# Kernel tuning notes

Measured on AMD Instinct MI355X. Metric: run time of the kernel, lower is better.

The kernel has to match this reference:

```python
import jax, jax.numpy as jnp
import numpy as np

NE = 14          # NUM_ELEMENTS
NC = 20          # world channels
CLONER = 13      # cloner element one-hot channel
CA = NE + 3      # cloner_assigns channel (=17)
B, H, W = 32, 256, 256

# torch.roll equivalents (dims 2 = H, dims 3 = W)
def _below(x):  return jnp.roll(x, -1, axis=2)
def _above(x):  return jnp.roll(x,  1, axis=2)
def _left(x):   return jnp.roll(x,  1, axis=3)
def _right(x):  return jnp.roll(x, -1, axis=3)
DIRS = (_below, _above, _left, _right)


def setup_inputs() -> dict:
    key = jax.random.key(0)
    k1, k2, k3, k4, k5 = jax.random.split(key, 5)
    # one-hot element channels [B, NE, H, W]
    ids = jax.random.randint(k1, (B, H, W), 0, NE)
    onehot = jnp.transpose(jax.nn.one_hot(ids, NE, dtype=jnp.float32), (0, 3, 1, 2))
    # extra scalar channels [B, NC-NE, H, W]
    extra = jax.random.normal(k2, (B, NC - NE, H, W), dtype=jnp.float32)
    world = jnp.concatenate([onehot, extra], axis=1)
    # cloner_assigns channel holds element ids stored as floats
    ca_init = jax.random.randint(k3, (B, 1, H, W), 0, NE).astype(jnp.float32)
    world = world.at[:, CA:CA + 1].set(ca_init)
    elem_vecs = jax.random.normal(k4, (NE, NC), dtype=jnp.float32)  # embedding table
    info = jax.random.normal(k5, (B,), dtype=jnp.float32)
    return {"world": world, "elem_vecs": elem_vecs, "info": info}


def _forward(world, elem_vecs):
    # labels = argmax over element one-hot channels, kept as [B,1,H,W]
    labels = jnp.argmax(world[:, :NE], axis=1)[:, None].astype(world.dtype)
    is_not_cloner = ~(world[:, CLONER:CLONER + 1] > 0.5)
    # Pass 1: sequentially propagate a label into empty cloner assignment slots.
    for d in DIRS:
        ca = world[:, CA:CA + 1]
        is_cloner_empty = (~is_not_cloner) & ((ca == 0.0) | (ca == 13.0))
        # torch: ~(is_cloner_empty|is_not_cloner)*ca + is_cloner_empty*dir_labels
        new_ca = jnp.where(is_cloner_empty, d(labels),
                           jnp.where(is_not_cloner, jnp.zeros((), world.dtype), ca))
        world = world.at[:, CA:CA + 1].set(new_ca)
    # Embedding lookup of assigned element vectors: [B,H,W,NC] -> [B,NC,H,W]
    vec = jnp.transpose(elem_vecs[world[:, CA].astype(jnp.int32)], (0, 3, 1, 2))
    # Pass 2: sequentially write cloner's element vector into adjacent empty cells.
    for d in DIRS:
        ca = world[:, CA:CA + 1]
        is_cloner = world[:, CLONER:CLONER + 1] > 0.5
        is_empty = world[:, 0:1] > 0.5
        mask = d(is_cloner & (ca != 0.0) & (ca != 13.0)) & is_empty  # [B,1,H,W]
        world = jnp.where(mask, d(vec), world)
    return world


def reference(world, elem_vecs, info):
    return (_forward(world, elem_vecs), info)
```

## Files before the change

### kernel.cpp

```cpp
#include <hip/hip_runtime.h>

namespace {
constexpr int kNE = 14;
constexpr int kNC = 20;
constexpr int kCloner = 13;
constexpr int kCA = 17;
constexpr int kB = 32;
constexpr int kH = 256;
constexpr int kW = 256;

constexpr int kSH = 4;
constexpr int kThreads = 256;
constexpr size_t kPlane = (size_t)kH * kW;

constexpr int kT = 32;
constexpr int kE = kT + 4;
constexpr int kLW = 40;
}


__global__ __launch_bounds__(kThreads)
void k_pack(const float* __restrict__ world, const float* __restrict__ info,
            float* __restrict__ out, unsigned char* __restrict__ pack)
{
    const int g = blockIdx.x * kThreads + threadIdx.x;
    const int b = g >> 14;
    const int rem = g & 16383;
    const size_t off = (size_t)rem << 2;
    const float* wb = world + (size_t)b * kNC * kPlane;

    int lab[4] = {0, 0, 0, 0};
    #pragma unroll
    for (int c = 0; c < kNE; ++c) {
        const float4 v = *reinterpret_cast<const float4*>(wb + (size_t)c * kPlane + off);
        if (v.x > 0.5f) lab[0] = c;
        if (v.y > 0.5f) lab[1] = c;
        if (v.z > 0.5f) lab[2] = c;
        if (v.w > 0.5f) lab[3] = c;
    }
    const float4 ca4 = *reinterpret_cast<const float4*>(wb + (size_t)kCA * kPlane + off);
    uchar4 p;
    p.x = (unsigned char)(lab[0] | ((int)ca4.x << 4));
    p.y = (unsigned char)(lab[1] | ((int)ca4.y << 4));
    p.z = (unsigned char)(lab[2] | ((int)ca4.z << 4));
    p.w = (unsigned char)(lab[3] | ((int)ca4.w << 4));
    *reinterpret_cast<uchar4*>(pack + (size_t)b * kPlane + off) = p;

    if (g < kB) out[(size_t)kB * kNC * kPlane + g] = info[g];
}

__device__ __forceinline__ unsigned bc_step(unsigned s, unsigned ns,
                                            const unsigned short* __restrict__ vb) {
    if ((ns & 2u) && (s & 1u)) {
        const unsigned v = (ns >> 4) & 15u;
        return (s & 0x00F0u) | vb[v] | (v << 8) | 0x1000u;
    }
    return s;
}

__global__ __launch_bounds__(kThreads)
void k_apply(const float* __restrict__ world, const float* __restrict__ ev,
             const unsigned char* __restrict__ pack, float* __restrict__ out)
{
    __shared__ unsigned char  sP[kSH + 4][kW];
    __shared__ unsigned short sA[kSH + 2][kW];
    __shared__ float sEV[kNE * kNC];
    __shared__ unsigned short sVbits[kNE];

    const int tid = threadIdx.x;
    const int y0 = blockIdx.x * kSH;
    const int b  = blockIdx.y;
    const float* wb = world + (size_t)b * kNC * kPlane;
    float*       ob = out   + (size_t)b * kNC * kPlane;
    const unsigned char* pb = pack + (size_t)b * kPlane;

    const int th   = tid >> 6;
    const int col4 = (tid & 63) * 4;
    const size_t off4 = (size_t)(y0 + th) * kW + col4;

    float4 extra[5];
    extra[0] = *reinterpret_cast<const float4*>(wb + (size_t)14 * kPlane + off4);
    extra[1] = *reinterpret_cast<const float4*>(wb + (size_t)15 * kPlane + off4);
    extra[2] = *reinterpret_cast<const float4*>(wb + (size_t)16 * kPlane + off4);
    extra[3] = *reinterpret_cast<const float4*>(wb + (size_t)18 * kPlane + off4);
    extra[4] = *reinterpret_cast<const float4*>(wb + (size_t)19 * kPlane + off4);

    for (int i = tid; i < kNE * kNC; i += kThreads) sEV[i] = ev[i];
    if (tid < kNE) {
        const float e0  = ev[tid * kNC + 0];
        const float c13 = ev[tid * kNC + kCloner];
        const float c17 = ev[tid * kNC + kCA];
        unsigned short vb = 0;
        if (e0 > 0.5f) vb |= 1;
        if (c13 > 0.5f && c17 != 0.0f && c17 != 13.0f) vb |= 2;
        sVbits[tid] = vb;
    }

    for (int idx = tid; idx < (kSH + 4) * (kW / 4); idx += kThreads) {
        const int r  = idx >> 6;
        const int c4 = (idx & 63) * 4;
        const int h  = (y0 - 2 + r) & (kH - 1);
        *reinterpret_cast<uchar4*>(&sP[r][c4]) =
            *reinterpret_cast<const uchar4*>(pb + (size_t)h * kW + c4);
    }
    __syncthreads();

    for (int idx = tid; idx < (kSH + 2) * kW; idx += kThreads) {
        const int r   = idx >> 8;
        const int col = idx & 255;
        const int pr  = r + 1;
        const unsigned p  = sP[pr][col];
        const unsigned lb = p & 15u;
        int fca = 0;
        if (lb == kCloner) {
            int ca = (int)(p >> 4);
            if (ca == 0 || ca == 13) ca = sP[pr + 1][col] & 15;
            if (ca == 0 || ca == 13) ca = sP[pr - 1][col] & 15;
            if (ca == 0 || ca == 13) ca = sP[pr][(col - 1) & 255] & 15;
            if (ca == 0 || ca == 13) ca = sP[pr][(col + 1) & 255] & 15;
            fca = ca;
        }
        unsigned short s = (unsigned short)(fca << 4);
        if (lb == 0) s |= 1;
        if (lb == kCloner && fca != 0 && fca != 13) s |= 2;
        sA[r][col] = s;
    }
    __syncthreads();

    const int ar = th + 1;
    unsigned s0[3][6];
    #pragma unroll
    for (int r = 0; r < 3; ++r)
        #pragma unroll
        for (int c = 0; c < 6; ++c)
            s0[r][c] = sA[ar - 1 + r][(col4 - 1 + c) & 255];

    unsigned s1[2][6];
    #pragma unroll
    for (int r = 0; r < 2; ++r)
        #pragma unroll
        for (int c = 0; c < 6; ++c)
            s1[r][c] = bc_step(s0[r][c], s0[r + 1][c], sVbits);

    unsigned s2[6];
    #pragma unroll
    for (int c = 0; c < 6; ++c)
        s2[c] = bc_step(s1[1][c], s1[0][c], sVbits);

    unsigned s3[5];
    #pragma unroll
    for (int c = 0; c < 5; ++c)
        s3[c] = bc_step(s2[c + 1], s2[c], sVbits);

    unsigned s4[4];
    #pragma unroll
    for (int j = 0; j < 4; ++j)
        s4[j] = bc_step(s3[j], s3[j + 1], sVbits);

    bool  o[4]; int src[4]; float fcaf[4]; int lb[4];
    #pragma unroll
    for (int j = 0; j < 4; ++j) {
        o[j]    = (s4[j] & 0x1000u) != 0;
        src[j]  = (s4[j] >> 8) & 15;
        fcaf[j] = (float)((s4[j] >> 4) & 15);
        lb[j]   = sP[th + 2][col4 + j] & 15;
    }

    #pragma unroll
    for (int c = 0; c < kNC; ++c) {
        float base[4];
        if (c < kNE) {
            #pragma unroll
            for (int j = 0; j < 4; ++j) base[j] = (lb[j] == c) ? 1.0f : 0.0f;
        } else if (c == kCA) {
            #pragma unroll
            for (int j = 0; j < 4; ++j) base[j] = fcaf[j];
        } else {
            const float4 v = extra[c < kCA ? c - kNE : c - kNE - 1];
            base[0] = v.x; base[1] = v.y; base[2] = v.z; base[3] = v.w;
        }
        float4 r;
        r.x = o[0] ? sEV[src[0] * kNC + c] : base[0];
        r.y = o[1] ? sEV[src[1] * kNC + c] : base[1];
        r.z = o[2] ? sEV[src[2] * kNC + c] : base[2];
        r.w = o[3] ? sEV[src[3] * kNC + c] : base[3];
        *reinterpret_cast<float4*>(ob + (size_t)c * kPlane + off4) = r;
    }
}

__global__ __launch_bounds__(kThreads)
void bc_fused(const float* __restrict__ world, const float* __restrict__ ev,
              const float* __restrict__ info, float* __restrict__ out)
{
    __shared__ unsigned short sPack[kE][kLW];
    __shared__ unsigned short sA[kE][kLW];
    __shared__ unsigned short sB[kE][kLW];
    __shared__ float sEV[kNE * kNC];
    __shared__ unsigned short sVbits[kNE];

    const int tid = threadIdx.x;
    const int b  = blockIdx.z;
    const int h0 = blockIdx.y * kT;
    const int w0 = blockIdx.x * kT;
    const float* wb = world + (size_t)b * kNC * kPlane;
    float*       ob = out   + (size_t)b * kNC * kPlane;

    for (int i = tid; i < kNE * kNC; i += kThreads) sEV[i] = ev[i];
    if (tid < kNE) {
        const float e0  = ev[tid * kNC + 0];
        const float c13 = ev[tid * kNC + kCloner];
        const float c17 = ev[tid * kNC + kCA];
        unsigned short vb = 0;
        if (e0 > 0.5f) vb |= 1;
        if (c13 > 0.5f && c17 != 0.0f && c17 != 13.0f) vb |= 2;
        sVbits[tid] = vb;
    }
    for (int idx = tid; idx < kE * 10; idx += kThreads) {
        const int eh = idx / 10;
        const int k  = idx - eh * 10;
        const int h = (h0 + eh - 2) & (kH - 1);
        const int w = (w0 - 4 + 4 * k) & (kW - 1);
        const size_t off = (size_t)h * kW + w;
        int lab[4] = {0,0,0,0};
        #pragma unroll
        for (int c = 0; c < kNE; ++c) {
            const float4 v = *reinterpret_cast<const float4*>(wb + (size_t)c * kPlane + off);
            if (v.x > 0.5f) lab[0] = c;
            if (v.y > 0.5f) lab[1] = c;
            if (v.z > 0.5f) lab[2] = c;
            if (v.w > 0.5f) lab[3] = c;
        }
        const float4 ca4 = *reinterpret_cast<const float4*>(wb + (size_t)kCA * kPlane + off);
        const int cai[4] = {(int)ca4.x, (int)ca4.y, (int)ca4.z, (int)ca4.w};
        #pragma unroll
        for (int j = 0; j < 4; ++j) {
            unsigned short p = (unsigned short)(lab[j] | (cai[j] << 8));
            if (lab[j] == kCloner) p |= 16;
            if (lab[j] == 0)       p |= 32;
            sPack[eh][4 * k + j] = p;
        }
    }
    __syncthreads();
    for (int idx = tid; idx < 34 * 34; idx += kThreads) {
        const int eh = idx / 34 + 1;
        const int lw = idx % 34 + 3;
        const unsigned short p = sPack[eh][lw];
        int fca = 0;
        if (p & 16) {
            int ca = (p >> 8) & 15;
            if (ca == 0 || ca == 13) ca = sPack[eh + 1][lw] & 15;
            if (ca == 0 || ca == 13) ca = sPack[eh - 1][lw] & 15;
            if (ca == 0 || ca == 13) ca = sPack[eh][lw - 1] & 15;
            if (ca == 0 || ca == 13) ca = sPack[eh][lw + 1] & 15;
            fca = ca;
        }
        unsigned short s = (unsigned short)(fca << 4);
        if (p & 32) s |= 1;
        if ((p & 16) && fca != 0 && fca != 13) s |= 2;
        sA[eh][lw] = s;
    }
    unsigned short (*prev)[kLW] = sA;
    unsigned short (*next)[kLW] = sB;
    {
        const int dh[4]   = {1, -1, 0, 0};
        const int dw[4]   = {0, 0, -1, 1};
        const int rhlo[4] = {1, 2, 2, 2};
        const int rhhi[4] = {33, 33, 33, 33};
        const int rwlo[4] = {3, 3, 4, 4};
        const int rwhi[4] = {36, 36, 36, 35};
        for (int d = 0; d < 4; ++d) {
            __syncthreads();
            const int nh = rhhi[d] - rhlo[d] + 1;
            const int nw = rwhi[d] - rwlo[d] + 1;
            for (int idx = tid; idx < nh * nw; idx += kThreads) {
                const int eh = rhlo[d] + idx / nw;
                const int lw = rwlo[d] + idx % nw;
                unsigned short s = prev[eh][lw];
                const unsigned short ns = prev[eh + dh[d]][lw + dw[d]];
                if ((ns & 2) && (s & 1)) {
                    const int v = (ns >> 4) & 15;
                    s = (unsigned short)((s & 0x00F0) | sVbits[v] | (v << 8) | 0x1000);
                }
                next[eh][lw] = s;
            }
            unsigned short (*t)[kLW] = prev; prev = next; next = t;
        }
    }
    __syncthreads();
    {
        const int th = tid >> 3;
        const int tw = (tid & 7) * 4;
        const int eh = th + 2;
        const size_t off = (size_t)(h0 + th) * kW + (w0 + tw);
        bool  o[4]; int src[4]; float fcaf[4]; int lb[4];
        #pragma unroll
        for (int j = 0; j < 4; ++j) {
            const unsigned short s = prev[eh][tw + 4 + j];
            o[j]    = (s & 0x1000) != 0;
            src[j]  = (s >> 8) & 15;
            fcaf[j] = (float)((s >> 4) & 15);
            lb[j]   = sPack[eh][tw + 4 + j] & 15;
        }
        #pragma unroll
        for (int c = 0; c < kNC; ++c) {
            float base[4];
            if (c >= kNE && c != kCA) {
                const float4 v = *reinterpret_cast<const float4*>(wb + (size_t)c * kPlane + off);
                base[0] = v.x; base[1] = v.y; base[2] = v.z; base[3] = v.w;
            } else if (c == kCA) {
                base[0] = fcaf[0]; base[1] = fcaf[1]; base[2] = fcaf[2]; base[3] = fcaf[3];
            } else {
                #pragma unroll
                for (int j = 0; j < 4; ++j) base[j] = (lb[j] == c) ? 1.0f : 0.0f;
            }
            float4 r;
            r.x = o[0] ? sEV[src[0] * kNC + c] : base[0];
            r.y = o[1] ? sEV[src[1] * kNC + c] : base[1];
            r.z = o[2] ? sEV[src[2] * kNC + c] : base[2];
            r.w = o[3] ? sEV[src[3] * kNC + c] : base[3];
            *reinterpret_cast<float4*>(ob + (size_t)c * kPlane + off) = r;
        }
    }
    if (blockIdx.x == 0 && blockIdx.y == 0 && blockIdx.z == 0 && tid < kB) {
        out[(size_t)kB * kNC * kPlane + tid] = info[tid];
    }
}

extern "C" void kernel_launch(void* const* d_in, const int* in_sizes, int n_in,
                              void* d_out, int out_size, void* d_ws, size_t ws_size,
                              hipStream_t stream) {
    const float* world = (const float*)d_in[0];
    const float* ev    = (const float*)d_in[1];
    const float* info  = (const float*)d_in[2];
    float* out = (float*)d_out;
    const size_t packBytes = (size_t)kB * kPlane;
    if (ws_size >= packBytes) {
        unsigned char* pack = (unsigned char*)d_ws;
        k_pack<<<dim3((kB * (int)kPlane / 4) / kThreads), kThreads, 0, stream>>>(world, info, out, pack);
        k_apply<<<dim3(kH / kSH, kB), kThreads, 0, stream>>>(world, ev, pack, out);
    } else {
        bc_fused<<<dim3(kW / kT, kH / kT, kB), kThreads, 0, stream>>>(world, ev, info, out);
    }
}
```

Before: 69.31 us.

## Split apply kernel into two channel-group launches with scattered overrides

Splits k_apply into two template instances. One writes the one-hot label channels and the cloner-assign channel, the other copies the five scalar extra channels. Overridden cells are now patched afterwards with scalar scattered stores instead of per-channel selects. The intent is to cut register pressure and raise occupancy in each kernel. In exchange, both launches recompute the stencil propagation and reload shared memory, and the scattered patch stores cause partial-line writes.

```diff
diff --git a/kernel.cpp b/kernel.cpp
--- a/kernel.cpp
+++ b/kernel.cpp
@@ -58,6 +58,7 @@
     return s;
 }
 
+template <int MODE>
 __global__ __launch_bounds__(kThreads)
 void k_apply(const float* __restrict__ world, const float* __restrict__ ev,
              const unsigned char* __restrict__ pack, float* __restrict__ out)
@@ -79,11 +80,13 @@
     const size_t off4 = (size_t)(y0 + th) * kW + col4;
 
     float4 extra[5];
-    extra[0] = *reinterpret_cast<const float4*>(wb + (size_t)14 * kPlane + off4);
-    extra[1] = *reinterpret_cast<const float4*>(wb + (size_t)15 * kPlane + off4);
-    extra[2] = *reinterpret_cast<const float4*>(wb + (size_t)16 * kPlane + off4);
-    extra[3] = *reinterpret_cast<const float4*>(wb + (size_t)18 * kPlane + off4);
-    extra[4] = *reinterpret_cast<const float4*>(wb + (size_t)19 * kPlane + off4);
+    if (MODE == 1) {
+        extra[0] = *reinterpret_cast<const float4*>(wb + (size_t)14 * kPlane + off4);
+        extra[1] = *reinterpret_cast<const float4*>(wb + (size_t)15 * kPlane + off4);
+        extra[2] = *reinterpret_cast<const float4*>(wb + (size_t)16 * kPlane + off4);
+        extra[3] = *reinterpret_cast<const float4*>(wb + (size_t)18 * kPlane + off4);
+        extra[4] = *reinterpret_cast<const float4*>(wb + (size_t)19 * kPlane + off4);
+    }
 
     for (int i = tid; i < kNE * kNC; i += kThreads) sEV[i] = ev[i];
     if (tid < kNE) {
@@ -157,34 +160,51 @@
     for (int j = 0; j < 4; ++j)
         s4[j] = bc_step(s3[j], s3[j + 1], sVbits);
 
-    bool  o[4]; int src[4]; float fcaf[4]; int lb[4];
-    #pragma unroll
-    for (int j = 0; j < 4; ++j) {
-        o[j]    = (s4[j] & 0x1000u) != 0;
-        src[j]  = (s4[j] >> 8) & 15;
-        fcaf[j] = (float)((s4[j] >> 4) & 15);
-        lb[j]   = sP[th + 2][col4 + j] & 15;
-    }
-
-    #pragma unroll
-    for (int c = 0; c < kNC; ++c) {
-        float base[4];
-        if (c < kNE) {
-            #pragma unroll
-            for (int j = 0; j < 4; ++j) base[j] = (lb[j] == c) ? 1.0f : 0.0f;
-        } else if (c == kCA) {
-            #pragma unroll
-            for (int j = 0; j < 4; ++j) base[j] = fcaf[j];
-        } else {
-            const float4 v = extra[c < kCA ? c - kNE : c - kNE - 1];
-            base[0] = v.x; base[1] = v.y; base[2] = v.z; base[3] = v.w;
-        }
-        float4 r;
-        r.x = o[0] ? sEV[src[0] * kNC + c] : base[0];
-        r.y = o[1] ? sEV[src[1] * kNC + c] : base[1];
-        r.z = o[2] ? sEV[src[2] * kNC + c] : base[2];
-        r.w = o[3] ? sEV[src[3] * kNC + c] : base[3];
-        *reinterpret_cast<float4*>(ob + (size_t)c * kPlane + off4) = r;
+    if (MODE == 0) {
+        int lb[4]; float fcaf[4];
+        #pragma unroll
+        for (int j = 0; j < 4; ++j) {
+            lb[j]   = sP[th + 2][col4 + j] & 15;
+            fcaf[j] = (float)((s4[j] >> 4) & 15);
+        }
+        #pragma unroll
+        for (int c = 0; c < kNE; ++c) {
+            float4 r;
+            r.x = (lb[0] == c) ? 1.0f : 0.0f;
+            r.y = (lb[1] == c) ? 1.0f : 0.0f;
+            r.z = (lb[2] == c) ? 1.0f : 0.0f;
+            r.w = (lb[3] == c) ? 1.0f : 0.0f;
+            *reinterpret_cast<float4*>(ob + (size_t)c * kPlane + off4) = r;
+        }
+        {
+            float4 r; r.x = fcaf[0]; r.y = fcaf[1]; r.z = fcaf[2]; r.w = fcaf[3];
+            *reinterpret_cast<float4*>(ob + (size_t)kCA * kPlane + off4) = r;
+        }
+        #pragma unroll
+        for (int j = 0; j < 4; ++j) {
+            if (s4[j] & 0x1000u) {
+                const float* vv = &sEV[((s4[j] >> 8) & 15) * kNC];
+                float* op = ob + off4 + j;
+                #pragma unroll
+                for (int c = 0; c < kNE; ++c) op[(size_t)c * kPlane] = vv[c];
+                op[(size_t)kCA * kPlane] = vv[kCA];
+            }
+        }
+    } else {
+        const int chans[5] = {14, 15, 16, 18, 19};
+        #pragma unroll
+        for (int k = 0; k < 5; ++k) {
+            *reinterpret_cast<float4*>(ob + (size_t)chans[k] * kPlane + off4) = extra[k];
+        }
+        #pragma unroll
+        for (int j = 0; j < 4; ++j) {
+            if (s4[j] & 0x1000u) {
+                const float* vv = &sEV[((s4[j] >> 8) & 15) * kNC];
+                float* op = ob + off4 + j;
+                #pragma unroll
+                for (int k = 0; k < 5; ++k) op[(size_t)chans[k] * kPlane] = vv[chans[k]];
+            }
+        }
     }
 }
 
@@ -337,7 +357,8 @@
     if (ws_size >= packBytes) {
         unsigned char* pack = (unsigned char*)d_ws;
         k_pack<<<dim3((kB * (int)kPlane / 4) / kThreads), kThreads, 0, stream>>>(world, info, out, pack);
-        k_apply<<<dim3(kH / kSH, kB), kThreads, 0, stream>>>(world, ev, pack, out);
+        k_apply<0><<<dim3(kH / kSH, kB), kThreads, 0, stream>>>(world, ev, pack, out);
+        k_apply<1><<<dim3(kH / kSH, kB), kThreads, 0, stream>>>(world, ev, pack, out);
     } else {
         bc_fused<<<dim3(kW / kT, kH / kT, kB), kThreads, 0, stream>>>(world, ev, info, out);
     }
```

New measurement: 103.9 us. +49.9%, slower.

## Split apply into state computation and per-channel expand kernels with XCD mapping

Applied to the files above, without the earlier changes.

Replaces the single apply kernel with two kernels. The first computes a packed 16-bit per-cell state (override flag, source id, assignment, label) into workspace. The second expands that state into all 20 output channels, with one block per (batch, channel, quarter-plane) and block indices swizzled so batches map to XCDs. The aim is better write locality and parallelism for the output stage, at the cost of an extra kernel launch, a 4MB state round trip through memory, and a larger workspace requirement.

```diff
diff --git a/kernel.cpp b/kernel.cpp
--- a/kernel.cpp
+++ b/kernel.cpp
@@ -59,33 +59,22 @@
 }
 
 __global__ __launch_bounds__(kThreads)
-void k_apply(const float* __restrict__ world, const float* __restrict__ ev,
-             const unsigned char* __restrict__ pack, float* __restrict__ out)
+void k_state(const float* __restrict__ ev, const unsigned char* __restrict__ pack,
+             unsigned short* __restrict__ state)
 {
     __shared__ unsigned char  sP[kSH + 4][kW];
     __shared__ unsigned short sA[kSH + 2][kW];
-    __shared__ float sEV[kNE * kNC];
     __shared__ unsigned short sVbits[kNE];
 
     const int tid = threadIdx.x;
     const int y0 = blockIdx.x * kSH;
     const int b  = blockIdx.y;
-    const float* wb = world + (size_t)b * kNC * kPlane;
-    float*       ob = out   + (size_t)b * kNC * kPlane;
     const unsigned char* pb = pack + (size_t)b * kPlane;
 
     const int th   = tid >> 6;
     const int col4 = (tid & 63) * 4;
     const size_t off4 = (size_t)(y0 + th) * kW + col4;
 
-    float4 extra[5];
-    extra[0] = *reinterpret_cast<const float4*>(wb + (size_t)14 * kPlane + off4);
-    extra[1] = *reinterpret_cast<const float4*>(wb + (size_t)15 * kPlane + off4);
-    extra[2] = *reinterpret_cast<const float4*>(wb + (size_t)16 * kPlane + off4);
-    extra[3] = *reinterpret_cast<const float4*>(wb + (size_t)18 * kPlane + off4);
-    extra[4] = *reinterpret_cast<const float4*>(wb + (size_t)19 * kPlane + off4);
-
-    for (int i = tid; i < kNE * kNC; i += kThreads) sEV[i] = ev[i];
     if (tid < kNE) {
         const float e0  = ev[tid * kNC + 0];
         const float c13 = ev[tid * kNC + kCloner];
@@ -157,34 +146,62 @@
     for (int j = 0; j < 4; ++j)
         s4[j] = bc_step(s3[j], s3[j + 1], sVbits);
 
-    bool  o[4]; int src[4]; float fcaf[4]; int lb[4];
-    #pragma unroll
-    for (int j = 0; j < 4; ++j) {
-        o[j]    = (s4[j] & 0x1000u) != 0;
-        src[j]  = (s4[j] >> 8) & 15;
-        fcaf[j] = (float)((s4[j] >> 4) & 15);
-        lb[j]   = sP[th + 2][col4 + j] & 15;
-    }
-
-    #pragma unroll
-    for (int c = 0; c < kNC; ++c) {
-        float base[4];
+    ushort4 st;
+    st.x = (unsigned short)((s4[0] & 0x1FF0u) | (sP[th + 2][col4 + 0] & 15u));
+    st.y = (unsigned short)((s4[1] & 0x1FF0u) | (sP[th + 2][col4 + 1] & 15u));
+    st.z = (unsigned short)((s4[2] & 0x1FF0u) | (sP[th + 2][col4 + 2] & 15u));
+    st.w = (unsigned short)((s4[3] & 0x1FF0u) | (sP[th + 2][col4 + 3] & 15u));
+    *reinterpret_cast<ushort4*>(state + (size_t)b * kPlane + off4) = st;
+}
+
+__global__ __launch_bounds__(kThreads)
+void k_expand(const float* __restrict__ world, const float* __restrict__ ev,
+              const unsigned short* __restrict__ state, float* __restrict__ out)
+{
+    __shared__ float sEV[kNE * kNC];
+
+    const int bid   = blockIdx.x;
+    const int xcd   = bid & 7;
+    const int inner = bid >> 3;
+    const int q     = inner & 3;
+    const int t2    = inner >> 2;
+    const int c     = t2 % kNC;
+    const int bhi   = t2 / kNC;
+    const int b     = xcd + 8 * bhi;
+
+    const int tid = threadIdx.x;
+    for (int i = tid; i < kNE * kNC; i += kThreads) sEV[i] = ev[i];
+    __syncthreads();
+
+    const unsigned short* sb = state + (size_t)b * kPlane;
+    const float* wp = world + ((size_t)b * kNC + c) * kPlane;
+    float*       op = out   + ((size_t)b * kNC + c) * kPlane;
+
+    #pragma unroll 4
+    for (int k = 0; k < 16; ++k) {
+        const size_t off = (size_t)(q * 4096 + (k << 8) + tid) << 2;
+        const ushort4 st = *reinterpret_cast<const ushort4*>(sb + off);
+        const unsigned s[4] = {st.x, st.y, st.z, st.w};
+        float4 r;
+        float* rp = &r.x;
         if (c < kNE) {
             #pragma unroll
-            for (int j = 0; j < 4; ++j) base[j] = (lb[j] == c) ? 1.0f : 0.0f;
+            for (int j = 0; j < 4; ++j)
+                rp[j] = (s[j] & 0x1000u) ? sEV[((s[j] >> 8) & 15) * kNC + c]
+                                         : (((s[j] & 15u) == (unsigned)c) ? 1.0f : 0.0f);
         } else if (c == kCA) {
             #pragma unroll
-            for (int j = 0; j < 4; ++j) base[j] = fcaf[j];
+            for (int j = 0; j < 4; ++j)
+                rp[j] = (s[j] & 0x1000u) ? sEV[((s[j] >> 8) & 15) * kNC + c]
+                                         : (float)((s[j] >> 4) & 15);
         } else {
-            const float4 v = extra[c < kCA ? c - kNE : c - kNE - 1];
-            base[0] = v.x; base[1] = v.y; base[2] = v.z; base[3] = v.w;
-        }
-        float4 r;
-        r.x = o[0] ? sEV[src[0] * kNC + c] : base[0];
-        r.y = o[1] ? sEV[src[1] * kNC + c] : base[1];
-        r.z = o[2] ? sEV[src[2] * kNC + c] : base[2];
-        r.w = o[3] ? sEV[src[3] * kNC + c] : base[3];
-        *reinterpret_cast<float4*>(ob + (size_t)c * kPlane + off4) = r;
+            const float4 in = *reinterpret_cast<const float4*>(wp + off);
+            const float* ip = &in.x;
+            #pragma unroll
+            for (int j = 0; j < 4; ++j)
+                rp[j] = (s[j] & 0x1000u) ? sEV[((s[j] >> 8) & 15) * kNC + c] : ip[j];
+        }
+        *reinterpret_cast<float4*>(op + off) = r;
     }
 }
 
@@ -333,11 +350,14 @@
     const float* ev    = (const float*)d_in[1];
     const float* info  = (const float*)d_in[2];
     float* out = (float*)d_out;
-    const size_t packBytes = (size_t)kB * kPlane;
-    if (ws_size >= packBytes) {
-        unsigned char* pack = (unsigned char*)d_ws;
+    const size_t packBytes  = (size_t)kB * kPlane;
+    const size_t stateBytes = (size_t)kB * kPlane * sizeof(unsigned short);
+    if (ws_size >= packBytes + stateBytes) {
+        unsigned char*  pack  = (unsigned char*)d_ws;
+        unsigned short* state = (unsigned short*)((char*)d_ws + packBytes);
         k_pack<<<dim3((kB * (int)kPlane / 4) / kThreads), kThreads, 0, stream>>>(world, info, out, pack);
-        k_apply<<<dim3(kH / kSH, kB), kThreads, 0, stream>>>(world, ev, pack, out);
+        k_state<<<dim3(kH / kSH, kB), kThreads, 0, stream>>>(ev, pack, state);
+        k_expand<<<dim3(kB * kNC * 4), kThreads, 0, stream>>>(world, ev, state, out);
     } else {
         bc_fused<<<dim3(kW / kT, kH / kT, kB), kThreads, 0, stream>>>(world, ev, info, out);
     }
```

After: 103.2 us. +48.8%, slower.
